# Performance work log

Measured on AMD Instinct MI355X. Metric: run time of the kernel, lower is better.

## Reference

```python
import jax, jax.numpy as jnp
import numpy as np

B = 4096
N_ENTITY = 100000
N_USER = 10000
N_RELATION = 32
DIM = 64
N_ITER = 2
K = 16  # n_neighbors


def setup_inputs() -> dict:
    key = jax.random.key(0)
    ks = jax.random.split(key, 8)
    pairs = jax.random.randint(ks[0], (B, 2), 0, N_USER, dtype=jnp.int64 if jax.config.jax_enable_x64 else jnp.int32)
    adj_entity = jax.random.randint(ks[1], (N_ENTITY, K), 0, N_ENTITY)
    adj_relation = jax.random.randint(ks[2], (N_ENTITY, K), 0, N_RELATION)
    # xavier_uniform-style scale for embeddings
    def xavier(k, shape):
        limit = float(np.sqrt(6.0 / (shape[0] + shape[1])))
        return jax.random.uniform(k, shape, jnp.float32, -limit, limit)
    entity_emb = xavier(ks[3], (N_ENTITY, DIM))
    relation_emb = xavier(ks[4], (N_RELATION, DIM))
    user_emb = xavier(ks[5], (N_USER, DIM))
    W = xavier(ks[6], (DIM, DIM))
    b = jnp.zeros((DIM,), jnp.float32)
    return {"pairs": pairs, "adj_entity": adj_entity, "adj_relation": adj_relation,
            "entity_emb": entity_emb, "relation_emb": relation_emb,
            "user_emb": user_emb, "W": W, "b": b}


def reference(pairs, adj_entity, adj_relation, entity_emb, relation_emb, user_emb, W, b):
    n = pairs.shape[0]
    dim = entity_emb.shape[1]
    k = adj_entity.shape[1]
    users = pairs[:, 0]
    items = pairs[:, 1]

    # multi-hop neighbor expansion (mirrors get_neighbors)
    entities = [items]
    relations = []
    for i in range(N_ITER):
        entities.append(adj_entity[entities[i]].reshape(-1))
        relations.append(adj_relation[entities[i]].reshape(-1))

    u = user_emb[users]  # [B, D]
    ev = [entity_emb[entities[i]].reshape(n, -1, dim) for i in range(N_ITER + 1)]
    rv = [relation_emb[relations[i]].reshape(n, -1, dim) for i in range(N_ITER)]

    for l in range(N_ITER):
        nxt = []
        for i in range(N_ITER - l):
            r = rv[i].reshape(n, -1, k, dim)          # [B, M, K, D]
            scores = jnp.einsum('bd,bmkd->bmk', u, r) # user-relation attention
            attn = jax.nn.softmax(scores, axis=-1)[..., None]
            nbr = (attn * ev[i + 1].reshape(n, -1, k, dim)).sum(axis=-2)  # [B, M, D]
            x = ev[i].reshape(n, -1, dim) + nbr       # residual add
            h = x @ W.T + b                            # Linear(dim, dim)
            nxt.append(jnp.tanh(h) if l == N_ITER - 1 else jax.nn.relu(h))
        ev = nxt

    item_embeddings = ev[0].reshape(-1, dim)  # [B, D]
    return jax.nn.sigmoid(jnp.sum(u * item_embeddings, axis=1))
```

## Files before the change

### kernel.cpp

```cpp
#include <hip/hip_runtime.h>
#include <hip/hip_bf16.h>
#include <math.h>

#define DIM  64
#define KN   16
#define NREL 32

__device__ __forceinline__ float frcp(float x) { return __builtin_amdgcn_rcpf(x); }

__device__ __forceinline__ unsigned short f2bf(float f) {
    unsigned u = __float_as_uint(f);
    u = (u + 0x7fffu + ((u >> 16) & 1u)) >> 16;
    return (unsigned short)u;
}
__device__ __forceinline__ float bflo(unsigned v) { return __uint_as_float(v << 16); }
__device__ __forceinline__ float bfhi(unsigned v) { return __uint_as_float(v & 0xffff0000u); }

typedef __attribute__((ext_vector_type(8))) short bfrag;
typedef __attribute__((ext_vector_type(4))) float f32x4;

__global__ __launch_bounds__(256, 2) void we_kernel_mfma(
    const float* __restrict__ entity_emb,
    const float* __restrict__ W,
    unsigned short* __restrict__ WEb,
    int nRows)
{
    const int tid  = threadIdx.x;
    const int wave = tid >> 6;
    const int lane = tid & 63;
    const int c = lane & 15;
    const int g = lane >> 4;

    const int nTiles = (nRows + 15) >> 4;
    const int t0 = (blockIdx.x * 4 + wave) * 2;
    if (t0 >= nTiles) return;

    bfrag a[4][2];
    #pragma unroll
    for (int m = 0; m < 4; ++m) {
        #pragma unroll
        for (int ks = 0; ks < 2; ++ks) {
            const float4* ws = (const float4*)(W + (size_t)(16 * m + c) * DIM + 8 * g + 32 * ks);
            const float4 w0 = ws[0], w1 = ws[1];
            a[m][ks][0] = (short)f2bf(w0.x); a[m][ks][1] = (short)f2bf(w0.y);
            a[m][ks][2] = (short)f2bf(w0.z); a[m][ks][3] = (short)f2bf(w0.w);
            a[m][ks][4] = (short)f2bf(w1.x); a[m][ks][5] = (short)f2bf(w1.y);
            a[m][ks][6] = (short)f2bf(w1.z); a[m][ks][7] = (short)f2bf(w1.w);
        }
    }

    float4 pe[2][4];
    #pragma unroll
    for (int j = 0; j < 2; ++j) {
        const int t = (t0 + j < nTiles) ? (t0 + j) : 0;
        int row = 16 * t + c;
        if (row >= nRows) row = nRows - 1;
        const float4* src = (const float4*)(entity_emb + (size_t)row * DIM + 8 * g);
        pe[j][0] = src[0];
        pe[j][1] = src[1];
        pe[j][2] = src[8];
        pe[j][3] = src[9];
    }

    #pragma unroll
    for (int j = 0; j < 2; ++j) {
        const int t = t0 + j;
        if (t >= nTiles) continue;

        bfrag b0, b1;
        b0[0] = (short)f2bf(pe[j][0].x); b0[1] = (short)f2bf(pe[j][0].y);
        b0[2] = (short)f2bf(pe[j][0].z); b0[3] = (short)f2bf(pe[j][0].w);
        b0[4] = (short)f2bf(pe[j][1].x); b0[5] = (short)f2bf(pe[j][1].y);
        b0[6] = (short)f2bf(pe[j][1].z); b0[7] = (short)f2bf(pe[j][1].w);
        b1[0] = (short)f2bf(pe[j][2].x); b1[1] = (short)f2bf(pe[j][2].y);
        b1[2] = (short)f2bf(pe[j][2].z); b1[3] = (short)f2bf(pe[j][2].w);
        b1[4] = (short)f2bf(pe[j][3].x); b1[5] = (short)f2bf(pe[j][3].y);
        b1[6] = (short)f2bf(pe[j][3].z); b1[7] = (short)f2bf(pe[j][3].w);

        f32x4 acc[4];
        #pragma unroll
        for (int m = 0; m < 4; ++m) {
            f32x4 z = {0.f, 0.f, 0.f, 0.f};
            z = __builtin_amdgcn_mfma_f32_16x16x32_bf16(a[m][0], b0, z, 0, 0, 0);
            z = __builtin_amdgcn_mfma_f32_16x16x32_bf16(a[m][1], b1, z, 0, 0, 0);
            acc[m] = z;
        }

        const int erow = 16 * t + c;
        if (erow < nRows) {
            #pragma unroll
            for (int m = 0; m < 4; ++m) {
                const unsigned lo = (unsigned)f2bf(acc[m][0]) | ((unsigned)f2bf(acc[m][1]) << 16);
                const unsigned hi = (unsigned)f2bf(acc[m][2]) | ((unsigned)f2bf(acc[m][3]) << 16);
                *(uint2*)(WEb + (size_t)erow * DIM + 16 * m + 4 * g) = make_uint2(lo, hi);
            }
        }
    }
}

__global__ __launch_bounds__(256, 4) void kgcn_main(
    const int* __restrict__ pairs,
    const int* __restrict__ adjE,
    const int* __restrict__ adjR,
    const unsigned short* __restrict__ WEb,
    const float* __restrict__ relation_emb,
    const float* __restrict__ user_emb,
    const float* __restrict__ W,
    const float* __restrict__ bias,
    float* __restrict__ out,
    int nPairs)
{
    __shared__ float ev1_s[4][KN * DIM];
    __shared__ float xb_s[4][DIM];

    const int tid  = threadIdx.x;
    const int wave = tid >> 6;
    const int lane = tid & 63;
    const int p    = blockIdx.x * 4 + wave;
    if (p >= nPairs) return;

    float* ev1 = ev1_s[wave];
    float* xb  = xb_s[wave];

    const int qq = lane >> 4;
    const int c  = lane & 15;
    const int c4 = c * 4;

    const int user = pairs[2 * p + 0];
    const int item = pairs[2 * p + 1];

    const float4 b4 = *(const float4*)(bias + c4);
    const uint2* WEq = (const uint2*)WEb;

    int rk0 = 0, e1 = 0;
    if (lane < KN) {
        rk0 = adjR[(size_t)item * KN + lane];
        e1  = adjE[(size_t)item * KN + lane];
    }

    float acc;
    {
        const int r = lane >> 1, hlf = lane & 1;
        const float4* rel4 = (const float4*)(relation_emb + r * DIM + hlf * 32);
        const float4* u4   = (const float4*)(user_emb + (size_t)user * DIM + hlf * 32);
        float a0 = 0.f, a1 = 0.f;
        #pragma unroll
        for (int j = 0; j < 8; j += 2) {
            float4 a = rel4[j],      b = u4[j];
            float4 cc = rel4[j + 1], d = u4[j + 1];
            a0 += a.x*b.x + a.y*b.y + a.z*b.z + a.w*b.w;
            a1 += cc.x*d.x + cc.y*d.y + cc.z*d.z + cc.w*d.w;
        }
        acc = a0 + a1;
        acc += __shfl_xor(acc, 1);
    }

    const uint2 itemv = WEq[(size_t)item * 16 + c];
    uint2 h0v[4];
    #pragma unroll
    for (int k = 0; k < 4; ++k) {
        const int e = __shfl(e1, qq * 4 + k);
        h0v[k] = WEq[(size_t)(unsigned)e * 16 + c];
    }

    int rkA[4], ekA[4];
    #pragma unroll
    for (int s = 0; s < 4; ++s) {
        const int g = __shfl(e1, 4 * s + qq);
        rkA[s] = adjR[(size_t)(unsigned)g * KN + c];
        ekA[s] = adjE[(size_t)(unsigned)g * KN + c];
    }

    auto softmax16 = [&](float s) -> float {
        float mx = s;
        mx = fmaxf(mx, __shfl_xor(mx, 1));
        mx = fmaxf(mx, __shfl_xor(mx, 2));
        mx = fmaxf(mx, __shfl_xor(mx, 4));
        mx = fmaxf(mx, __shfl_xor(mx, 8));
        float e = __expf(s - mx);
        float ss = e;
        ss += __shfl_xor(ss, 1);
        ss += __shfl_xor(ss, 2);
        ss += __shfl_xor(ss, 4);
        ss += __shfl_xor(ss, 8);
        return e * frcp(ss);
    };

    float wA[4];
    #pragma unroll
    for (int s = 0; s < 4; ++s) wA[s] = softmax16(__shfl(acc, rkA[s] << 1));
    const float w0 = softmax16(__shfl(acc, rk0 << 1));

    #pragma unroll 2
    for (int s = 0; s < 4; ++s) {
        const int gm = 4 * s + qq;
        const int gs = __shfl(e1, gm);
        uint2 sv = WEq[(size_t)(unsigned)gs * 16 + c];
        float ax = b4.x + bflo(sv.x);
        float ay = b4.y + bfhi(sv.x);
        float az = b4.z + bflo(sv.y);
        float aw = b4.w + bfhi(sv.y);
        #pragma unroll
        for (int k = 0; k < KN; ++k) {
            const int   e = __shfl(ekA[s], qq * 16 + k);
            const float w = __shfl(wA[s],  qq * 16 + k);
            uint2 v = WEq[(size_t)(unsigned)e * 16 + c];
            ax += w * bflo(v.x);
            ay += w * bfhi(v.x);
            az += w * bflo(v.y);
            aw += w * bfhi(v.y);
        }
        *(float4*)&ev1[gm * DIM + c4] =
            make_float4(fmaxf(ax, 0.f), fmaxf(ay, 0.f), fmaxf(az, 0.f), fmaxf(aw, 0.f));
    }

    float ax = 0.f, ay = 0.f, az = 0.f, aw = 0.f;
    #pragma unroll
    for (int k = 0; k < 4; ++k) {
        const float w = __shfl(w0, qq * 4 + k);
        ax += w * bflo(h0v[k].x);
        ay += w * bfhi(h0v[k].x);
        az += w * bflo(h0v[k].y);
        aw += w * bfhi(h0v[k].y);
    }
    ax += __shfl_xor(ax, 16); ay += __shfl_xor(ay, 16);
    az += __shfl_xor(az, 16); aw += __shfl_xor(aw, 16);
    ax += __shfl_xor(ax, 32); ay += __shfl_xor(ay, 32);
    az += __shfl_xor(az, 32); aw += __shfl_xor(aw, 32);
    ax += bflo(itemv.x) + b4.x;
    ay += bfhi(itemv.x) + b4.y;
    az += bflo(itemv.y) + b4.z;
    aw += bfhi(itemv.y) + b4.w;
    const float e0x = fmaxf(ax, 0.f), e0y = fmaxf(ay, 0.f);
    const float e0z = fmaxf(az, 0.f), e0w = fmaxf(aw, 0.f);

    asm volatile("s_waitcnt lgkmcnt(0)" ::: "memory");
    float sx = 0.f, sy = 0.f, sz = 0.f, sw = 0.f;
    #pragma unroll
    for (int k = 0; k < 4; ++k) {
        const int   kg = qq * 4 + k;
        const float w  = __shfl(w0, kg);
        float4 ev = *(const float4*)&ev1[kg * DIM + c4];
        sx += w * ev.x;
        sy += w * ev.y;
        sz += w * ev.z;
        sw += w * ev.w;
    }
    sx += __shfl_xor(sx, 16); sy += __shfl_xor(sy, 16);
    sz += __shfl_xor(sz, 16); sw += __shfl_xor(sw, 16);
    sx += __shfl_xor(sx, 32); sy += __shfl_xor(sy, 32);
    sz += __shfl_xor(sz, 32); sw += __shfl_xor(sw, 32);

    asm volatile("s_waitcnt lgkmcnt(0)" ::: "memory");
    if (qq == 0)
        *(float4*)&xb[c4] = make_float4(e0x + sx, e0y + sy, e0z + sz, e0w + sw);
    asm volatile("s_waitcnt lgkmcnt(0)" ::: "memory");
    float h0 = bias[lane], h1 = 0.f, h2 = 0.f, h3 = 0.f;
    {
        const float4* Wl  = (const float4*)(W + lane * DIM);
        const float4* xv4 = (const float4*)xb;
        #pragma unroll
        for (int j = 0; j < 16; j += 4) {
            float4 w0v = Wl[j],   x0v = xv4[j];
            float4 w1v = Wl[j+1], x1v = xv4[j+1];
            float4 w2v = Wl[j+2], x2v = xv4[j+2];
            float4 w3v = Wl[j+3], x3v = xv4[j+3];
            h0 += w0v.x*x0v.x + w0v.y*x0v.y + w0v.z*x0v.z + w0v.w*x0v.w;
            h1 += w1v.x*x1v.x + w1v.y*x1v.y + w1v.z*x1v.z + w1v.w*x1v.w;
            h2 += w2v.x*x2v.x + w2v.y*x2v.y + w2v.z*x2v.z + w2v.w*x2v.w;
            h3 += w3v.x*x3v.x + w3v.y*x3v.y + w3v.z*x3v.z + w3v.w*x3v.w;
        }
    }
    const float itemf = tanhf((h0 + h1) + (h2 + h3));

    float d = user_emb[(size_t)user * DIM + lane] * itemf;
    d += __shfl_xor(d, 1);
    d += __shfl_xor(d, 2);
    d += __shfl_xor(d, 4);
    d += __shfl_xor(d, 8);
    d += __shfl_xor(d, 16);
    d += __shfl_xor(d, 32);
    if (lane == 0) out[p] = 1.f / (1.f + expf(-d));
}

__global__ __launch_bounds__(256, 4) void kgcn_fallback(
    const int* __restrict__ pairs, const int* __restrict__ adj_entity,
    const int* __restrict__ adj_relation, const float* __restrict__ entity_emb,
    const float* __restrict__ relation_emb, const float* __restrict__ user_emb,
    const float* __restrict__ W, const float* __restrict__ bias,
    float* __restrict__ out, int nPairs)
{
    __shared__ float ev1_s[2][KN * DIM];
    __shared__ float xb_s[4][DIM];
    const int tid = threadIdx.x, wave = tid >> 6, lane = tid & 63;
    const int q = wave >> 1, half = wave & 1;
    int p = blockIdx.x * 2 + q;
    if (p >= nPairs) p = nPairs - 1;
    float* ev1 = ev1_s[q]; float* xb = xb_s[wave];
    const int user = pairs[2 * p + 0], item = pairs[2 * p + 1];
    const float bval = bias[lane];
    const float* emb_l = entity_emb + lane;
    const float4* W4 = (const float4*)(W + lane * DIM);
    int rk0 = 0, e1 = 0;
    if (lane < KN) {
        rk0 = adj_relation[(size_t)item * KN + lane];
        e1  = adj_entity[(size_t)item * KN + lane];
    }
    float acc;
    {
        const int r = lane >> 1, hlf = lane & 1;
        const float4* rel4 = (const float4*)(relation_emb + r * DIM + hlf * 32);
        const float4* u4 = (const float4*)(user_emb + (size_t)user * DIM + hlf * 32);
        float a0 = 0.f, a1 = 0.f;
        #pragma unroll
        for (int j = 0; j < 8; j += 2) {
            float4 a = rel4[j], b = u4[j], c = rel4[j+1], d = u4[j+1];
            a0 += a.x*b.x + a.y*b.y + a.z*b.z + a.w*b.w;
            a1 += c.x*d.x + c.y*d.y + c.z*d.z + c.w*d.w;
        }
        acc = a0 + a1; acc += __shfl_xor(acc, 1);
    }
    auto softmax16 = [&](float s) -> float {
        float mx = s;
        mx = fmaxf(mx, __shfl_xor(mx, 1)); mx = fmaxf(mx, __shfl_xor(mx, 2));
        mx = fmaxf(mx, __shfl_xor(mx, 4)); mx = fmaxf(mx, __shfl_xor(mx, 8));
        float e = __expf(s - mx);
        float ss = e;
        ss += __shfl_xor(ss, 1); ss += __shfl_xor(ss, 2);
        ss += __shfl_xor(ss, 4); ss += __shfl_xor(ss, 8);
        return e * frcp(ss);
    };
    auto matvec = [&](float xv) -> float {
        asm volatile("s_waitcnt lgkmcnt(0)" ::: "memory");
        xb[lane] = xv;
        asm volatile("s_waitcnt lgkmcnt(0)" ::: "memory");
        float h0 = bval, h1 = 0.f, h2 = 0.f, h3 = 0.f;
        const float4* xv4 = (const float4*)xb;
        #pragma unroll
        for (int j = 0; j < 16; j += 4) {
            float4 w0 = W4[j], x0 = xv4[j], w1 = W4[j+1], x1 = xv4[j+1];
            float4 w2 = W4[j+2], x2 = xv4[j+2], w3 = W4[j+3], x3 = xv4[j+3];
            h0 += w0.x*x0.x + w0.y*x0.y + w0.z*x0.z + w0.w*x0.w;
            h1 += w1.x*x1.x + w1.y*x1.y + w1.z*x1.z + w1.w*x1.w;
            h2 += w2.x*x2.x + w2.y*x2.y + w2.z*x2.z + w2.w*x2.w;
            h3 += w3.x*x3.x + w3.y*x3.y + w3.z*x3.z + w3.w*x3.w;
        }
        return (h0 + h1) + (h2 + h3);
    };
    auto gather = [&](int self, int ek, float w) -> float {
        float xa = emb_l[(size_t)(unsigned)self * DIM], xc = 0.f;
        #pragma unroll
        for (int k = 0; k < KN; k += 2) {
            const int e0i = __shfl(ek, k); const float f0 = __shfl(w, k);
            const int e1i = __shfl(ek, k + 1); const float f1 = __shfl(w, k + 1);
            xa += f0 * emb_l[(size_t)(unsigned)e0i * DIM];
            xc += f1 * emb_l[(size_t)(unsigned)e1i * DIM];
        }
        return xa + xc;
    };
    int rk_n = 0, ek_n = 0;
    {
        const int g0 = __shfl(e1, half * 8);
        if (lane < KN) {
            rk_n = adj_relation[(size_t)(unsigned)g0 * KN + lane];
            ek_n = adj_entity[(size_t)(unsigned)g0 * KN + lane];
        }
    }
    #pragma unroll 1
    for (int mi = 0; mi < 8; ++mi) {
        const int m = half * 8 + mi;
        const int g = __shfl(e1, m);
        const int rk = rk_n, ek = ek_n;
        if (mi + 1 < 8) {
            const int gn = __shfl(e1, m + 1);
            if (lane < KN) {
                rk_n = adj_relation[(size_t)(unsigned)gn * KN + lane];
                ek_n = adj_entity[(size_t)(unsigned)gn * KN + lane];
            }
        }
        const float w = softmax16(__shfl(acc, rk << 1));
        const float x = gather(g, ek, w);
        ev1[m * DIM + lane] = fmaxf(matvec(x), 0.f);
    }
    __syncthreads();
    if (half != 0) return;
    const float w0 = softmax16(__shfl(acc, rk0 << 1));
    const float x0 = gather(item, e1, w0);
    const float e0 = fmaxf(matvec(x0), 0.f);
    float xa = e0, xc = 0.f;
    #pragma unroll
    for (int k = 0; k < KN; k += 2) {
        xa += __shfl(w0, k) * ev1[k * DIM + lane];
        xc += __shfl(w0, k + 1) * ev1[(k + 1) * DIM + lane];
    }
    const float itemf = tanhf(matvec(xa + xc));
    float d = user_emb[(size_t)user * DIM + lane] * itemf;
    d += __shfl_xor(d, 1); d += __shfl_xor(d, 2); d += __shfl_xor(d, 4);
    d += __shfl_xor(d, 8); d += __shfl_xor(d, 16); d += __shfl_xor(d, 32);
    if (lane == 0) out[p] = 1.f / (1.f + expf(-d));
}

extern "C" void kernel_launch(void* const* d_in, const int* in_sizes, int n_in,
                              void* d_out, int out_size, void* d_ws, size_t ws_size,
                              hipStream_t stream) {
    const int*   pairs        = (const int*)d_in[0];
    const int*   adj_entity   = (const int*)d_in[1];
    const int*   adj_relation = (const int*)d_in[2];
    const float* entity_emb   = (const float*)d_in[3];
    const float* relation_emb = (const float*)d_in[4];
    const float* user_emb     = (const float*)d_in[5];
    const float* W            = (const float*)d_in[6];
    const float* b            = (const float*)d_in[7];
    float* out = (float*)d_out;

    const int nPairs = in_sizes[0] / 2;
    const int nEnt   = in_sizes[3] / DIM;
    const size_t weBytes = (size_t)in_sizes[3] * sizeof(unsigned short);

    if (ws_size >= weBytes) {
        unsigned short* WEb = (unsigned short*)d_ws;
        const int nTiles = (nEnt + 15) >> 4;
        const int preBlocks = (nTiles + 7) / 8;
        we_kernel_mfma<<<preBlocks, 256, 0, stream>>>(entity_emb, W, WEb, nEnt);
        const int mainBlocks = (nPairs + 3) / 4;
        kgcn_main<<<mainBlocks, 256, 0, stream>>>(pairs, adj_entity, adj_relation,
                                                  WEb, relation_emb, user_emb,
                                                  W, b, out, nPairs);
    } else {
        const int nBlocks = (nPairs + 1) / 2;
        kgcn_fallback<<<nBlocks, 256, 0, stream>>>(pairs, adj_entity, adj_relation,
                                                   entity_emb, relation_emb, user_emb,
                                                   W, b, out, nPairs);
    }
}
```

Baseline: 128.7 us.

## Prefetch second-hop neighbor embeddings into registers before softmax and accumulation

```diff
diff --git a/kernel.cpp b/kernel.cpp
--- a/kernel.cpp
+++ b/kernel.cpp
@@ -98,7 +98,7 @@
     }
 }
 
-__global__ __launch_bounds__(256, 4) void kgcn_main(
+__global__ __launch_bounds__(256, 3) void kgcn_main(
     const int* __restrict__ pairs,
     const int* __restrict__ adjE,
     const int* __restrict__ adjR,
@@ -138,21 +138,13 @@
         e1  = adjE[(size_t)item * KN + lane];
     }
 
-    float acc;
+    float4 rr[8], ur[8];
     {
         const int r = lane >> 1, hlf = lane & 1;
         const float4* rel4 = (const float4*)(relation_emb + r * DIM + hlf * 32);
         const float4* u4   = (const float4*)(user_emb + (size_t)user * DIM + hlf * 32);
-        float a0 = 0.f, a1 = 0.f;
-        #pragma unroll
-        for (int j = 0; j < 8; j += 2) {
-            float4 a = rel4[j],      b = u4[j];
-            float4 cc = rel4[j + 1], d = u4[j + 1];
-            a0 += a.x*b.x + a.y*b.y + a.z*b.z + a.w*b.w;
-            a1 += cc.x*d.x + cc.y*d.y + cc.z*d.z + cc.w*d.w;
-        }
-        acc = a0 + a1;
-        acc += __shfl_xor(acc, 1);
+        #pragma unroll
+        for (int j = 0; j < 8; ++j) { rr[j] = rel4[j]; ur[j] = u4[j]; }
     }
 
     const uint2 itemv = WEq[(size_t)item * 16 + c];
@@ -162,14 +154,40 @@
         const int e = __shfl(e1, qq * 4 + k);
         h0v[k] = WEq[(size_t)(unsigned)e * 16 + c];
     }
-
-    int rkA[4], ekA[4];
+    int rkA[4], ekA[4], gsA[4];
     #pragma unroll
     for (int s = 0; s < 4; ++s) {
-        const int g = __shfl(e1, 4 * s + qq);
-        rkA[s] = adjR[(size_t)(unsigned)g * KN + c];
-        ekA[s] = adjE[(size_t)(unsigned)g * KN + c];
-    }
+        gsA[s] = __shfl(e1, 4 * s + qq);
+        rkA[s] = adjR[(size_t)(unsigned)gsA[s] * KN + c];
+        ekA[s] = adjE[(size_t)(unsigned)gsA[s] * KN + c];
+    }
+
+    float acc;
+    {
+        float a0 = 0.f, a1 = 0.f;
+        #pragma unroll
+        for (int j = 0; j < 8; j += 2) {
+            float4 a = rr[j],     b = ur[j];
+            float4 cc = rr[j+1],  d = ur[j+1];
+            a0 += a.x*b.x + a.y*b.y + a.z*b.z + a.w*b.w;
+            a1 += cc.x*d.x + cc.y*d.y + cc.z*d.z + cc.w*d.w;
+        }
+        acc = a0 + a1;
+        acc += __shfl_xor(acc, 1);
+    }
+
+    uint2 svA[4];
+    uint2 nvA[3][KN];
+    #pragma unroll
+    for (int s = 0; s < 3; ++s) {
+        svA[s] = WEq[(size_t)(unsigned)gsA[s] * 16 + c];
+        #pragma unroll
+        for (int k = 0; k < KN; ++k) {
+            const int e = __shfl(ekA[s], qq * 16 + k);
+            nvA[s][k] = WEq[(size_t)(unsigned)e * 16 + c];
+        }
+    }
+    svA[3] = WEq[(size_t)(unsigned)gsA[3] * 16 + c];
 
     auto softmax16 = [&](float s) -> float {
         float mx = s;
@@ -191,26 +209,62 @@
     for (int s = 0; s < 4; ++s) wA[s] = softmax16(__shfl(acc, rkA[s] << 1));
     const float w0 = softmax16(__shfl(acc, rk0 << 1));
 
-    #pragma unroll 2
-    for (int s = 0; s < 4; ++s) {
-        const int gm = 4 * s + qq;
-        const int gs = __shfl(e1, gm);
-        uint2 sv = WEq[(size_t)(unsigned)gs * 16 + c];
-        float ax = b4.x + bflo(sv.x);
-        float ay = b4.y + bfhi(sv.x);
-        float az = b4.z + bflo(sv.y);
-        float aw = b4.w + bfhi(sv.y);
+    {
+        float ax = b4.x + bflo(svA[0].x);
+        float ay = b4.y + bfhi(svA[0].x);
+        float az = b4.z + bflo(svA[0].y);
+        float aw = b4.w + bfhi(svA[0].y);
         #pragma unroll
         for (int k = 0; k < KN; ++k) {
-            const int   e = __shfl(ekA[s], qq * 16 + k);
-            const float w = __shfl(wA[s],  qq * 16 + k);
-            uint2 v = WEq[(size_t)(unsigned)e * 16 + c];
+            const float w = __shfl(wA[0], qq * 16 + k);
+            uint2 v = nvA[0][k];
             ax += w * bflo(v.x);
             ay += w * bfhi(v.x);
             az += w * bflo(v.y);
             aw += w * bfhi(v.y);
         }
-        *(float4*)&ev1[gm * DIM + c4] =
+        *(float4*)&ev1[qq * DIM + c4] =
+            make_float4(fmaxf(ax, 0.f), fmaxf(ay, 0.f), fmaxf(az, 0.f), fmaxf(aw, 0.f));
+    }
+    uint2 nv3[KN];
+    #pragma unroll
+    for (int k = 0; k < KN; ++k) {
+        const int e = __shfl(ekA[3], qq * 16 + k);
+        nv3[k] = WEq[(size_t)(unsigned)e * 16 + c];
+    }
+    #pragma unroll
+    for (int s = 1; s < 3; ++s) {
+        float ax = b4.x + bflo(svA[s].x);
+        float ay = b4.y + bfhi(svA[s].x);
+        float az = b4.z + bflo(svA[s].y);
+        float aw = b4.w + bfhi(svA[s].y);
+        #pragma unroll
+        for (int k = 0; k < KN; ++k) {
+            const float w = __shfl(wA[s], qq * 16 + k);
+            uint2 v = nvA[s][k];
+            ax += w * bflo(v.x);
+            ay += w * bfhi(v.x);
+            az += w * bflo(v.y);
+            aw += w * bfhi(v.y);
+        }
+        *(float4*)&ev1[(4 * s + qq) * DIM + c4] =
+            make_float4(fmaxf(ax, 0.f), fmaxf(ay, 0.f), fmaxf(az, 0.f), fmaxf(aw, 0.f));
+    }
+    {
+        float ax = b4.x + bflo(svA[3].x);
+        float ay = b4.y + bfhi(svA[3].x);
+        float az = b4.z + bflo(svA[3].y);
+        float aw = b4.w + bfhi(svA[3].y);
+        #pragma unroll
+        for (int k = 0; k < KN; ++k) {
+            const float w = __shfl(wA[3], qq * 16 + k);
+            uint2 v = nv3[k];
+            ax += w * bflo(v.x);
+            ay += w * bfhi(v.x);
+            az += w * bflo(v.y);
+            aw += w * bfhi(v.y);
+        }
+        *(float4*)&ev1[(12 + qq) * DIM + c4] =
             make_float4(fmaxf(ax, 0.f), fmaxf(ay, 0.f), fmaxf(az, 0.f), fmaxf(aw, 0.f));
     }
 
```

After: 128.2 us. Within noise of the previous version (-0.4%).
